# Kernel tuning notes

Hardware: AMD Instinct MI355X
Metric: run time of the kernel (lower is better)

The kernel has to match this reference:

```python
import jax, jax.numpy as jnp
import numpy as np
import math

B = 1024
INPUT_SHAPE = (8, 8, 8, 8)
OUTPUT_SHAPE = (8, 8, 8, 8)
RANK_SHAPE = (2, 2, 2, 2)
BLOCK_NUM = 4
OUTPUT_SIZE = int(np.prod(OUTPUT_SHAPE))
CORE_SIZE = int(np.prod(RANK_SHAPE))


def setup_inputs() -> dict:
    key = jax.random.key(0)
    k1, k2, k3 = jax.random.split(key, 3)
    stdv = 1.0 / math.sqrt(OUTPUT_SIZE)  # reset_parameters: uniform(-stdv, stdv)
    inputs = jax.random.normal(k1, (B, int(np.prod(INPUT_SHAPE))), dtype=jnp.float32)
    # core_block{b}: shape rank_shape; factor{j}_block{b}: shape (I_j, O_j, R_j)
    cores = jax.random.uniform(k2, (BLOCK_NUM,) + RANK_SHAPE, minval=-stdv, maxval=stdv, dtype=jnp.float32)
    factors = jax.random.uniform(
        k3, (BLOCK_NUM, len(RANK_SHAPE), INPUT_SHAPE[0], OUTPUT_SHAPE[0], RANK_SHAPE[0]),
        minval=-stdv, maxval=stdv, dtype=jnp.float32)
    return {"inputs": inputs, "cores": cores, "factors": factors}


def reference(inputs, cores, factors):
    Bn = inputs.shape[0]
    # view(-1, *input_shape) then permute(0, n, n-1, ..., 1)
    x = inputs.reshape(Bn, *INPUT_SHAPE)
    x = jnp.transpose(x, (0, 4, 3, 2, 1))  # [B, i3, i2, i1, i0]
    res = jnp.zeros((Bn, OUTPUT_SIZE), dtype=inputs.dtype)
    for b in range(BLOCK_NUM):
        cal = x
        factor_offset = 1
        for j in range(len(RANK_SHAPE)):
            f = factors[b, j]            # (I, J, R)
            I, J, R = f.shape
            cal = cal.reshape(-1, I) @ f.reshape(I, J * R)
            cal = cal.reshape(Bn * factor_offset, -1, J * R)
            cal = jnp.transpose(cal, (0, 2, 1))
            factor_offset *= J
        # contract with core flattened row-major (exactly as core.view(core_size, -1))
        cal = cal.reshape(-1, CORE_SIZE) @ cores[b].reshape(CORE_SIZE, 1)
        res = res + cal.reshape(Bn, -1)
    return res
```

## Files before the change

### kernel.cpp

```cpp
#include <hip/hip_runtime.h>
#include <hip/hip_bf16.h>
#include <stdint.h>

typedef __attribute__((ext_vector_type(8))) __bf16 bf16x8;
typedef __attribute__((ext_vector_type(4))) float f32x4;
typedef __attribute__((ext_vector_type(8))) unsigned short u16x8;

__device__ __forceinline__ unsigned short f2bf(float f) {
    unsigned u = __builtin_bit_cast(unsigned, f);
    return (unsigned short)((u + 0x7fffu + ((u >> 16) & 1u)) >> 16);
}

__device__ __forceinline__ void glds16(const void* g, void* l) {
    __builtin_amdgcn_global_load_lds(
        (const __attribute__((address_space(1))) unsigned int*)(uintptr_t)g,
        (__attribute__((address_space(3))) unsigned int*)l, 16, 0, 0);
}

#define VMCNT(n) asm volatile("s_waitcnt vmcnt(" #n ")" ::: "memory")
#define BAR()                                  \
    do {                                       \
        asm volatile("" ::: "memory");         \
        __builtin_amdgcn_s_barrier();          \
        asm volatile("" ::: "memory");         \
    } while (0)

__global__ __launch_bounds__(256) void prep_fused(const float* __restrict__ factors,
                                                  const float* __restrict__ cores,
                                                  const float4* __restrict__ xin,
                                                  ushort4* __restrict__ xb,
                                                  unsigned short* __restrict__ Wt) {
    if (blockIdx.x >= 1024) {
        int i = (blockIdx.x - 1024) * 256 + threadIdx.x;
        float4 v = xin[i];
        ushort4 o;
        o.x = f2bf(v.x); o.y = f2bf(v.y); o.z = f2bf(v.z); o.w = f2bf(v.w);
        xb[i] = o;
        return;
    }
    __shared__ unsigned short As2[256 * 40];
    __shared__ unsigned short Bs2[64 * 40];
    __shared__ unsigned short lbuf[4 * 64 * 72];
    const int tid = threadIdx.x, lane = tid & 63, w = tid >> 6;
    const int bo = blockIdx.x >> 6, bn4 = (blockIdx.x >> 2) & 15, wn = blockIdx.x & 3;

    {
        int o01 = bo * 4 + (tid >> 6), a01 = tid & 63;
        int o0 = o01 >> 3, o1 = o01 & 7, a0 = a01 >> 3, a1 = a01 & 7;
#pragma unroll
        for (int k = 0; k < 16; ++k) {
            int b = k >> 2, q = k & 3, r0 = q >> 1, r1 = q & 1;
            float v = factors[b*512 +   0 + a0*16 + o0*2 + r0]
                    * factors[b*512 + 128 + a1*16 + o1*2 + r1];
            As2[tid * 40 + k] = f2bf(v);
            As2[tid * 40 + 16 + k] = 0;
        }
    }
    {
        int o23 = bn4 * 4 + wn, o2 = o23 >> 3, o3 = o23 & 7;
#pragma unroll
        for (int rep = 0; rep < 4; ++rep) {
            int task = rep * 256 + tid;
            int n = task >> 4, k = task & 15;
            int a2 = n >> 3, a3 = n & 7;
            int b = k >> 2, q = k & 3, r0 = q >> 1, r1 = q & 1;
            float s = 0.f;
#pragma unroll
            for (int r2 = 0; r2 < 2; ++r2)
#pragma unroll
                for (int r3 = 0; r3 < 2; ++r3)
                    s += factors[b*512 + 256 + a2*16 + o2*2 + r2]
                       * factors[b*512 + 384 + a3*16 + o3*2 + r3]
                       * cores[b*16 + r3*8 + r2*4 + r1*2 + r0];
            Bs2[n * 40 + k] = f2bf(s);
            Bs2[n * 40 + 16 + k] = 0;
        }
    }
    __syncthreads();

    const int fr = lane & 15, fh = lane >> 4;
    bf16x8 af[4], bf_[4];
#pragma unroll
    for (int mf = 0; mf < 4; ++mf)
        af[mf] = *(const bf16x8*)&As2[(w * 64 + mf * 16 + fr) * 40 + fh * 8];
#pragma unroll
    for (int nf = 0; nf < 4; ++nf)
        bf_[nf] = *(const bf16x8*)&Bs2[(nf * 16 + fr) * 40 + fh * 8];
    f32x4 acc[4][4] = {};
#pragma unroll
    for (int mf = 0; mf < 4; ++mf)
#pragma unroll
        for (int nf = 0; nf < 4; ++nf)
            acc[mf][nf] = __builtin_amdgcn_mfma_f32_16x16x32_bf16(
                af[mf], bf_[nf], acc[mf][nf], 0, 0, 0);
#pragma unroll
    for (int mf = 0; mf < 4; ++mf)
#pragma unroll
        for (int nf = 0; nf < 4; ++nf)
#pragma unroll
            for (int j = 0; j < 4; ++j)
                lbuf[w * 4608 + (mf * 16 + fh * 4 + j) * 72 + nf * 16 + fr] =
                    f2bf(acc[mf][nf][j]);
    const int o = (bo * 4 + w) * 64 + bn4 * 4 + wn;
    unsigned short* dst = Wt + (size_t)o * 4096;
#pragma unroll
    for (int i = 0; i < 8; ++i) {
        int c = i * 64 + lane;
        *(u16x8*)&dst[c * 8] =
            *(const u16x8*)&lbuf[w * 4608 + (c >> 3) * 72 + (c & 7) * 8];
    }
}

__global__ __launch_bounds__(256, 2) void gemm_bt64(const unsigned short* __restrict__ A,
                                                    const unsigned short* __restrict__ Bt,
                                                    float* __restrict__ C) {
    constexpr int K = 4096;
    constexpr int N = 4096;
    constexpr int BK = 64;
    constexpr int NT = K / BK;
    __shared__ alignas(16) char lds[3][24576];
    const int tid = threadIdx.x;
    const int lane = tid & 63, w = tid >> 6;
    const int wm = w >> 1, wn = w & 1;
    const int xcd = blockIdx.x & 7, r = blockIdx.x >> 3;
    const int bn = xcd * 4 + (r & 3);
    const int bm = r >> 2;

    const unsigned short* gA[2]; const unsigned short* gB[4];
    int lAoff[2], lBoff[4];
#pragma unroll
    for (int i = 0; i < 2; ++i) {
        int cs = i * 256 + tid;
        int row = cs >> 3;
        int c = (cs & 7) ^ ((row >> 1) & 7);
        gA[i] = A + (size_t)(bm * 64 + row) * K + c * 8;
        lAoff[i] = i * 4096 + w * 1024;
    }
#pragma unroll
    for (int i = 0; i < 4; ++i) {
        int cs = i * 256 + tid;
        int row = cs >> 3;
        int c = (cs & 7) ^ ((row >> 1) & 7);
        gB[i] = Bt + (size_t)(bn * 128 + row) * K + c * 8;
        lBoff[i] = 8192 + i * 4096 + w * 1024;
    }

#define STAGE(buf, kt)                                                        \
    do {                                                                      \
        _Pragma("unroll")                                                     \
        for (int i = 0; i < 2; ++i) glds16(gA[i] + (kt), &lds[buf][lAoff[i]]);\
        _Pragma("unroll")                                                     \
        for (int i = 0; i < 4; ++i) glds16(gB[i] + (kt), &lds[buf][lBoff[i]]);\
    } while (0)

    const int fr = lane & 15, fh = lane >> 4;
    const int sk = (fr >> 1) & 7;
    int aoff[2], boff[2];
#pragma unroll
    for (int kk = 0; kk < 2; ++kk) {
        aoff[kk] = (wm * 32 + fr) * 128 + (((kk * 4 + fh) ^ sk) << 4);
        boff[kk] = 8192 + (wn * 64 + fr) * 128 + (((kk * 4 + fh) ^ sk) << 4);
    }

    f32x4 acc[2][4] = {};

#define COMPUTE(buf)                                                          \
    do {                                                                      \
        const char* base = &lds[buf][0];                                      \
        _Pragma("unroll")                                                     \
        for (int kk = 0; kk < 2; ++kk) {                                      \
            bf16x8 af2[2], bf4[4];                                            \
            _Pragma("unroll")                                                 \
            for (int m = 0; m < 2; ++m)                                       \
                af2[m] = *(const bf16x8*)(base + aoff[kk] + m * 2048);        \
            _Pragma("unroll")                                                 \
            for (int n = 0; n < 4; ++n)                                       \
                bf4[n] = *(const bf16x8*)(base + boff[kk] + n * 2048);        \
            _Pragma("unroll")                                                 \
            for (int m = 0; m < 2; ++m)                                       \
                _Pragma("unroll")                                             \
                for (int n = 0; n < 4; ++n)                                   \
                    acc[m][n] = __builtin_amdgcn_mfma_f32_16x16x32_bf16(      \
                        af2[m], bf4[n], acc[m][n], 0, 0, 0);                  \
        }                                                                     \
    } while (0)

#define PHASE(tb, sbuf, cbuf)                                                 \
    do {                                                                      \
        STAGE(sbuf, ((tb) + 2) * BK);                                         \
        VMCNT(12);                                                            \
        BAR();                                                                \
        COMPUTE(cbuf);                                                        \
        BAR();                                                                \
    } while (0)

    STAGE(0, 0);
    STAGE(1, BK);
    for (int t = 0; t < 60; t += 3) {
        PHASE(t, 2, 0);
        PHASE(t + 1, 0, 1);
        PHASE(t + 2, 1, 2);
    }
    PHASE(60, 2, 0);
    PHASE(61, 0, 1);
    VMCNT(6);  BAR(); COMPUTE(2); BAR();
    VMCNT(0);  BAR(); COMPUTE(0);

    const int crow0 = bm * 64 + wm * 32 + fh * 4;
    const int ccol0 = bn * 128 + wn * 64 + fr;
#pragma unroll
    for (int m = 0; m < 2; ++m)
#pragma unroll
        for (int n = 0; n < 4; ++n)
#pragma unroll
            for (int j = 0; j < 4; ++j)
                C[(size_t)(crow0 + m * 16 + j) * N + (ccol0 + n * 16)] = acc[m][n][j];
#undef STAGE
#undef COMPUTE
#undef PHASE
}

extern "C" void kernel_launch(void* const* d_in, const int* in_sizes, int n_in,
                              void* d_out, int out_size, void* d_ws, size_t ws_size,
                              hipStream_t stream) {
    const float* inputs  = (const float*)d_in[0];
    const float* cores   = (const float*)d_in[1];
    const float* factors = (const float*)d_in[2];
    float* out = (float*)d_out;

    char* ws = (char*)d_ws;
    unsigned short* xb = (unsigned short*)ws;
    unsigned short* Wt = (unsigned short*)(ws + (8u << 20));

    prep_fused<<<5120, 256, 0, stream>>>(factors, cores,
                                         (const float4*)inputs, (ushort4*)xb, Wt);
    gemm_bt64<<<512, 256, 0, stream>>>(xb, Wt, out);
}
```

Baseline: 64.44 us.

## Load GEMM A-operand directly into registers and shrink LDS to double buffering

```diff
diff --git a/kernel.cpp b/kernel.cpp
--- a/kernel.cpp
+++ b/kernel.cpp
@@ -24,6 +24,8 @@
         __builtin_amdgcn_s_barrier();          \
         asm volatile("" ::: "memory");         \
     } while (0)
+
+#define MFMA16(a, b, c) __builtin_amdgcn_mfma_f32_16x16x32_bf16((a), (b), (c), 0, 0, 0)
 
 __global__ __launch_bounds__(256) void prep_fused(const float* __restrict__ factors,
                                                   const float* __restrict__ cores,
@@ -91,8 +93,7 @@
     for (int mf = 0; mf < 4; ++mf)
 #pragma unroll
         for (int nf = 0; nf < 4; ++nf)
-            acc[mf][nf] = __builtin_amdgcn_mfma_f32_16x16x32_bf16(
-                af[mf], bf_[nf], acc[mf][nf], 0, 0, 0);
+            acc[mf][nf] = MFMA16(af[mf], bf_[nf], acc[mf][nf]);
 #pragma unroll
     for (int mf = 0; mf < 4; ++mf)
 #pragma unroll
@@ -111,14 +112,13 @@
     }
 }
 
-__global__ __launch_bounds__(256, 2) void gemm_bt64(const unsigned short* __restrict__ A,
+__global__ __launch_bounds__(256, 2) void gemm_areg(const unsigned short* __restrict__ A,
                                                     const unsigned short* __restrict__ Bt,
                                                     float* __restrict__ C) {
     constexpr int K = 4096;
     constexpr int N = 4096;
     constexpr int BK = 64;
-    constexpr int NT = K / BK;
-    __shared__ alignas(16) char lds[3][24576];
+    __shared__ alignas(16) char lds[2][16384];
     const int tid = threadIdx.x;
     const int lane = tid & 63, w = tid >> 6;
     const int wm = w >> 1, wn = w & 1;
@@ -126,85 +126,81 @@
     const int bn = xcd * 4 + (r & 3);
     const int bm = r >> 2;
 
-    const unsigned short* gA[2]; const unsigned short* gB[4];
-    int lAoff[2], lBoff[4];
-#pragma unroll
-    for (int i = 0; i < 2; ++i) {
-        int cs = i * 256 + tid;
-        int row = cs >> 3;
-        int c = (cs & 7) ^ ((row >> 1) & 7);
-        gA[i] = A + (size_t)(bm * 64 + row) * K + c * 8;
-        lAoff[i] = i * 4096 + w * 1024;
-    }
+    const unsigned short* gB[4];
+    int lBoff[4];
 #pragma unroll
     for (int i = 0; i < 4; ++i) {
         int cs = i * 256 + tid;
         int row = cs >> 3;
         int c = (cs & 7) ^ ((row >> 1) & 7);
         gB[i] = Bt + (size_t)(bn * 128 + row) * K + c * 8;
-        lBoff[i] = 8192 + i * 4096 + w * 1024;
-    }
-
-#define STAGE(buf, kt)                                                        \
-    do {                                                                      \
-        _Pragma("unroll")                                                     \
-        for (int i = 0; i < 2; ++i) glds16(gA[i] + (kt), &lds[buf][lAoff[i]]);\
-        _Pragma("unroll")                                                     \
-        for (int i = 0; i < 4; ++i) glds16(gB[i] + (kt), &lds[buf][lBoff[i]]);\
+        lBoff[i] = i * 4096 + w * 1024;
+    }
+
+#define STAGEB(buf, tt)                                            \
+    do {                                                           \
+        glds16(gB[0] + (tt) * BK, &lds[buf][lBoff[0]]);            \
+        glds16(gB[1] + (tt) * BK, &lds[buf][lBoff[1]]);            \
+        glds16(gB[2] + (tt) * BK, &lds[buf][lBoff[2]]);            \
+        glds16(gB[3] + (tt) * BK, &lds[buf][lBoff[3]]);            \
     } while (0)
 
     const int fr = lane & 15, fh = lane >> 4;
+    const unsigned short* a00 = A + (size_t)(bm * 64 + wm * 32 + fr) * K + fh * 8;
+    const unsigned short* a01 = a00 + 32;
+    const unsigned short* a10 = a00 + (size_t)16 * K;
+    const unsigned short* a11 = a10 + 32;
+
+    bf16x8 aE00, aE01, aE10, aE11;
+    bf16x8 aO00, aO01, aO10, aO11;
+#define ALOAD(S, tt)                                               \
+    do {                                                           \
+        a##S##00 = *(const bf16x8*)(a00 + (tt) * BK);              \
+        a##S##01 = *(const bf16x8*)(a01 + (tt) * BK);              \
+        a##S##10 = *(const bf16x8*)(a10 + (tt) * BK);              \
+        a##S##11 = *(const bf16x8*)(a11 + (tt) * BK);              \
+    } while (0)
+
     const int sk = (fr >> 1) & 7;
-    int aoff[2], boff[2];
-#pragma unroll
-    for (int kk = 0; kk < 2; ++kk) {
-        aoff[kk] = (wm * 32 + fr) * 128 + (((kk * 4 + fh) ^ sk) << 4);
-        boff[kk] = 8192 + (wn * 64 + fr) * 128 + (((kk * 4 + fh) ^ sk) << 4);
-    }
+    const int boff0 = (wn * 64 + fr) * 128 + ((fh ^ sk) << 4);
+    const int boff1 = (wn * 64 + fr) * 128 + (((4 + fh) ^ sk) << 4);
 
     f32x4 acc[2][4] = {};
 
-#define COMPUTE(buf)                                                          \
-    do {                                                                      \
-        const char* base = &lds[buf][0];                                      \
-        _Pragma("unroll")                                                     \
-        for (int kk = 0; kk < 2; ++kk) {                                      \
-            bf16x8 af2[2], bf4[4];                                            \
-            _Pragma("unroll")                                                 \
-            for (int m = 0; m < 2; ++m)                                       \
-                af2[m] = *(const bf16x8*)(base + aoff[kk] + m * 2048);        \
-            _Pragma("unroll")                                                 \
-            for (int n = 0; n < 4; ++n)                                       \
-                bf4[n] = *(const bf16x8*)(base + boff[kk] + n * 2048);        \
-            _Pragma("unroll")                                                 \
-            for (int m = 0; m < 2; ++m)                                       \
-                _Pragma("unroll")                                             \
-                for (int n = 0; n < 4; ++n)                                   \
-                    acc[m][n] = __builtin_amdgcn_mfma_f32_16x16x32_bf16(      \
-                        af2[m], bf4[n], acc[m][n], 0, 0, 0);                  \
-        }                                                                     \
-    } while (0)
-
-#define PHASE(tb, sbuf, cbuf)                                                 \
-    do {                                                                      \
-        STAGE(sbuf, ((tb) + 2) * BK);                                         \
-        VMCNT(12);                                                            \
-        BAR();                                                                \
-        COMPUTE(cbuf);                                                        \
-        BAR();                                                                \
-    } while (0)
-
-    STAGE(0, 0);
-    STAGE(1, BK);
-    for (int t = 0; t < 60; t += 3) {
-        PHASE(t, 2, 0);
-        PHASE(t + 1, 0, 1);
-        PHASE(t + 2, 1, 2);
-    }
-    PHASE(60, 2, 0);
-    PHASE(61, 0, 1);
-    VMCNT(6);  BAR(); COMPUTE(2); BAR();
-    VMCNT(0);  BAR(); COMPUTE(0);
+#define CHALF(base, bof, A0, A1)                                   \
+    do {                                                           \
+        bf16x8 b0 = *(const bf16x8*)((base) + (bof));              \
+        bf16x8 b1 = *(const bf16x8*)((base) + (bof) + 2048);       \
+        bf16x8 b2 = *(const bf16x8*)((base) + (bof) + 4096);       \
+        bf16x8 b3 = *(const bf16x8*)((base) + (bof) + 6144);       \
+        acc[0][0] = MFMA16(A0, b0, acc[0][0]);                     \
+        acc[0][1] = MFMA16(A0, b1, acc[0][1]);                     \
+        acc[0][2] = MFMA16(A0, b2, acc[0][2]);                     \
+        acc[0][3] = MFMA16(A0, b3, acc[0][3]);                     \
+        acc[1][0] = MFMA16(A1, b0, acc[1][0]);                     \
+        acc[1][1] = MFMA16(A1, b1, acc[1][1]);                     \
+        acc[1][2] = MFMA16(A1, b2, acc[1][2]);                     \
+        acc[1][3] = MFMA16(A1, b3, acc[1][3]);                     \
+    } while (0)
+
+#define COMPUTE(buf, S)                                            \
+    do {                                                           \
+        const char* base_ = &lds[buf][0];                          \
+        CHALF(base_, boff0, a##S##00, a##S##10);                   \
+        CHALF(base_, boff1, a##S##01, a##S##11);                   \
+    } while (0)
+
+    ALOAD(E, 0);
+    STAGEB(0, 0);
+    for (int t = 0; t < 62; t += 2) {
+        ALOAD(O, t + 1); STAGEB(1, t + 1);
+        VMCNT(8); BAR(); COMPUTE(0, E); BAR();
+        ALOAD(E, t + 2); STAGEB(0, t + 2);
+        VMCNT(8); BAR(); COMPUTE(1, O); BAR();
+    }
+    ALOAD(O, 63); STAGEB(1, 63);
+    VMCNT(8); BAR(); COMPUTE(0, E); BAR();
+    VMCNT(0); BAR(); COMPUTE(1, O);
 
     const int crow0 = bm * 64 + wm * 32 + fh * 4;
     const int ccol0 = bn * 128 + wn * 64 + fr;
@@ -215,9 +211,10 @@
 #pragma unroll
             for (int j = 0; j < 4; ++j)
                 C[(size_t)(crow0 + m * 16 + j) * N + (ccol0 + n * 16)] = acc[m][n][j];
-#undef STAGE
+#undef STAGEB
+#undef ALOAD
+#undef CHALF
 #undef COMPUTE
-#undef PHASE
 }
 
 extern "C" void kernel_launch(void* const* d_in, const int* in_sizes, int n_in,
@@ -234,5 +231,5 @@
 
     prep_fused<<<5120, 256, 0, stream>>>(factors, cores,
                                          (const float4*)inputs, (ushort4*)xb, Wt);
-    gemm_bt64<<<512, 256, 0, stream>>>(xb, Wt, out);
-}
+    gemm_areg<<<512, 256, 0, stream>>>(xb, Wt, out);
+}
```

Result: slower. 103.6 us (+60.7%).

## Switch GEMM to 128x128 tiles with split-K of two plus reduction kernel

Applied to the files above, without the earlier changes.

```diff
diff --git a/kernel.cpp b/kernel.cpp
--- a/kernel.cpp
+++ b/kernel.cpp
@@ -24,6 +24,8 @@
         __builtin_amdgcn_s_barrier();          \
         asm volatile("" ::: "memory");         \
     } while (0)
+
+#define MFMA16(a, b, c) __builtin_amdgcn_mfma_f32_16x16x32_bf16((a), (b), (c), 0, 0, 0)
 
 __global__ __launch_bounds__(256) void prep_fused(const float* __restrict__ factors,
                                                   const float* __restrict__ cores,
@@ -91,8 +93,7 @@
     for (int mf = 0; mf < 4; ++mf)
 #pragma unroll
         for (int nf = 0; nf < 4; ++nf)
-            acc[mf][nf] = __builtin_amdgcn_mfma_f32_16x16x32_bf16(
-                af[mf], bf_[nf], acc[mf][nf], 0, 0, 0);
+            acc[mf][nf] = MFMA16(af[mf], bf_[nf], acc[mf][nf]);
 #pragma unroll
     for (int mf = 0; mf < 4; ++mf)
 #pragma unroll
@@ -111,91 +112,79 @@
     }
 }
 
-__global__ __launch_bounds__(256, 2) void gemm_bt64(const unsigned short* __restrict__ A,
-                                                    const unsigned short* __restrict__ Bt,
-                                                    float* __restrict__ C) {
+__global__ __launch_bounds__(256, 2) void gemm_128sk2(const unsigned short* __restrict__ A,
+                                                      const unsigned short* __restrict__ Bt,
+                                                      float* __restrict__ P) {
     constexpr int K = 4096;
     constexpr int N = 4096;
-    constexpr int BK = 64;
-    constexpr int NT = K / BK;
-    __shared__ alignas(16) char lds[3][24576];
+    constexpr int BK = 32;
+    constexpr int KCH = 2048;
+    __shared__ alignas(16) char lds[3][16384];
     const int tid = threadIdx.x;
     const int lane = tid & 63, w = tid >> 6;
     const int wm = w >> 1, wn = w & 1;
     const int xcd = blockIdx.x & 7, r = blockIdx.x >> 3;
     const int bn = xcd * 4 + (r & 3);
-    const int bm = r >> 2;
-
-    const unsigned short* gA[2]; const unsigned short* gB[4];
-    int lAoff[2], lBoff[4];
+    const int bm = (r >> 2) & 7;
+    const int ks = r >> 5;
+
+    const unsigned short* gA[2]; const unsigned short* gB[2];
+    int lAoff[2], lBoff[2];
 #pragma unroll
     for (int i = 0; i < 2; ++i) {
         int cs = i * 256 + tid;
-        int row = cs >> 3;
-        int c = (cs & 7) ^ ((row >> 1) & 7);
-        gA[i] = A + (size_t)(bm * 64 + row) * K + c * 8;
+        int row = cs >> 2;
+        int c = (cs & 3) ^ ((row >> 1) & 3);
+        gA[i] = A  + (size_t)(bm * 128 + row) * K + ks * KCH + c * 8;
+        gB[i] = Bt + (size_t)(bn * 128 + row) * K + ks * KCH + c * 8;
         lAoff[i] = i * 4096 + w * 1024;
-    }
-#pragma unroll
-    for (int i = 0; i < 4; ++i) {
-        int cs = i * 256 + tid;
-        int row = cs >> 3;
-        int c = (cs & 7) ^ ((row >> 1) & 7);
-        gB[i] = Bt + (size_t)(bn * 128 + row) * K + c * 8;
         lBoff[i] = 8192 + i * 4096 + w * 1024;
     }
 
-#define STAGE(buf, kt)                                                        \
-    do {                                                                      \
-        _Pragma("unroll")                                                     \
-        for (int i = 0; i < 2; ++i) glds16(gA[i] + (kt), &lds[buf][lAoff[i]]);\
-        _Pragma("unroll")                                                     \
-        for (int i = 0; i < 4; ++i) glds16(gB[i] + (kt), &lds[buf][lBoff[i]]);\
+#define STAGE(buf, tt)                                             \
+    do {                                                           \
+        glds16(gA[0] + (tt) * BK, &lds[buf][lAoff[0]]);            \
+        glds16(gA[1] + (tt) * BK, &lds[buf][lAoff[1]]);            \
+        glds16(gB[0] + (tt) * BK, &lds[buf][lBoff[0]]);            \
+        glds16(gB[1] + (tt) * BK, &lds[buf][lBoff[1]]);            \
     } while (0)
 
     const int fr = lane & 15, fh = lane >> 4;
-    const int sk = (fr >> 1) & 7;
-    int aoff[2], boff[2];
-#pragma unroll
-    for (int kk = 0; kk < 2; ++kk) {
-        aoff[kk] = (wm * 32 + fr) * 128 + (((kk * 4 + fh) ^ sk) << 4);
-        boff[kk] = 8192 + (wn * 64 + fr) * 128 + (((kk * 4 + fh) ^ sk) << 4);
-    }
-
-    f32x4 acc[2][4] = {};
+    const int xoff = (fh ^ ((fr >> 1) & 3)) << 4;
+    int aoff[4], boff[4];
+#pragma unroll
+    for (int m = 0; m < 4; ++m) aoff[m] = (wm * 64 + m * 16 + fr) * 64 + xoff;
+#pragma unroll
+    for (int n = 0; n < 4; ++n) boff[n] = 8192 + (wn * 64 + n * 16 + fr) * 64 + xoff;
+
+    f32x4 acc[4][4] = {};
 
 #define COMPUTE(buf)                                                          \
     do {                                                                      \
         const char* base = &lds[buf][0];                                      \
+        bf16x8 af[4], bf[4];                                                  \
         _Pragma("unroll")                                                     \
-        for (int kk = 0; kk < 2; ++kk) {                                      \
-            bf16x8 af2[2], bf4[4];                                            \
-            _Pragma("unroll")                                                 \
-            for (int m = 0; m < 2; ++m)                                       \
-                af2[m] = *(const bf16x8*)(base + aoff[kk] + m * 2048);        \
+        for (int m = 0; m < 4; ++m) af[m] = *(const bf16x8*)(base + aoff[m]); \
+        _Pragma("unroll")                                                     \
+        for (int n = 0; n < 4; ++n) bf[n] = *(const bf16x8*)(base + boff[n]); \
+        _Pragma("unroll")                                                     \
+        for (int m = 0; m < 4; ++m)                                           \
             _Pragma("unroll")                                                 \
             for (int n = 0; n < 4; ++n)                                       \
-                bf4[n] = *(const bf16x8*)(base + boff[kk] + n * 2048);        \
-            _Pragma("unroll")                                                 \
-            for (int m = 0; m < 2; ++m)                                       \
-                _Pragma("unroll")                                             \
-                for (int n = 0; n < 4; ++n)                                   \
-                    acc[m][n] = __builtin_amdgcn_mfma_f32_16x16x32_bf16(      \
-                        af2[m], bf4[n], acc[m][n], 0, 0, 0);                  \
-        }                                                                     \
+                acc[m][n] = MFMA16(af[m], bf[n], acc[m][n]);                  \
     } while (0)
 
 #define PHASE(tb, sbuf, cbuf)                                                 \
     do {                                                                      \
-        STAGE(sbuf, ((tb) + 2) * BK);                                         \
-        VMCNT(12);                                                            \
+        STAGE(sbuf, (tb) + 2);                                                \
+        VMCNT(8);                                                             \
         BAR();                                                                \
         COMPUTE(cbuf);                                                        \
         BAR();                                                                \
     } while (0)
 
     STAGE(0, 0);
-    STAGE(1, BK);
+    STAGE(1, 1);
     for (int t = 0; t < 60; t += 3) {
         PHASE(t, 2, 0);
         PHASE(t + 1, 0, 1);
@@ -203,21 +192,35 @@
     }
     PHASE(60, 2, 0);
     PHASE(61, 0, 1);
-    VMCNT(6);  BAR(); COMPUTE(2); BAR();
+    VMCNT(4);  BAR(); COMPUTE(2); BAR();
     VMCNT(0);  BAR(); COMPUTE(0);
 
-    const int crow0 = bm * 64 + wm * 32 + fh * 4;
+    float* Po = P + (size_t)ks * 4194304;
+    const int crow0 = bm * 128 + wm * 64 + fh * 4;
     const int ccol0 = bn * 128 + wn * 64 + fr;
 #pragma unroll
-    for (int m = 0; m < 2; ++m)
+    for (int m = 0; m < 4; ++m)
 #pragma unroll
         for (int n = 0; n < 4; ++n)
 #pragma unroll
             for (int j = 0; j < 4; ++j)
-                C[(size_t)(crow0 + m * 16 + j) * N + (ccol0 + n * 16)] = acc[m][n][j];
+                Po[(size_t)(crow0 + m * 16 + j) * N + (ccol0 + n * 16)] = acc[m][n][j];
 #undef STAGE
 #undef COMPUTE
 #undef PHASE
+}
+
+__global__ __launch_bounds__(256) void reduce2(const float4* __restrict__ P,
+                                               float4* __restrict__ C) {
+    int i = blockIdx.x * 256 + threadIdx.x;
+    float4 a = P[i];
+    float4 b = P[i + 1048576];
+    float4 o;
+    o.x = a.x + b.x;
+    o.y = a.y + b.y;
+    o.z = a.z + b.z;
+    o.w = a.w + b.w;
+    C[i] = o;
 }
 
 extern "C" void kernel_launch(void* const* d_in, const int* in_sizes, int n_in,
@@ -231,8 +234,10 @@
     char* ws = (char*)d_ws;
     unsigned short* xb = (unsigned short*)ws;
     unsigned short* Wt = (unsigned short*)(ws + (8u << 20));
+    float* Pp = (float*)(ws + (40u << 20));
 
     prep_fused<<<5120, 256, 0, stream>>>(factors, cores,
                                          (const float4*)inputs, (ushort4*)xb, Wt);
-    gemm_bt64<<<512, 256, 0, stream>>>(xb, Wt, out);
-}
+    gemm_128sk2<<<512, 256, 0, stream>>>(xb, Wt, Pp);
+    reduce2<<<4096, 256, 0, stream>>>((const float4*)Pp, (float4*)out);
+}
```

Measured after the change: 68.97 us. +7.0%, slower.
